# Optimization experiments

Hardware: AMD Instinct MI355X
Metric: run time of the kernel (lower is better)

## Reference

```python
import jax, jax.numpy as jnp
import numpy as np

NUM_HEADS = 6
TAU = 1.0


def _split_heads(y, h):
    b, n, c = y.shape
    return y.reshape(b, n, h, c // h).transpose(0, 2, 1, 3)  # b h n d


def setup_inputs() -> dict:
    key = jax.random.key(0)
    B, M, C = 8, 1026, 384
    names = ["Wq1", "Wq2", "Wk1", "Wk2", "Wv1", "Wv2", "Wo"]
    ks = jax.random.split(key, len(names) + 3)
    inp = {"x": jax.random.normal(ks[0], (B, M, C), jnp.float32)}
    for i, nm in enumerate(names):
        inp[nm] = jax.random.normal(ks[i + 1], (C, C), jnp.float32) * 0.02
        inp["b" + nm[1:]] = jnp.zeros((C,), jnp.float32)
    inp["weights"] = jax.random.normal(ks[-2], (4,), jnp.float32)
    u = jax.random.uniform(ks[-1], (4,), jnp.float32, 1e-6, 1.0 - 1e-6)
    inp["gumbel_noise"] = -jnp.log(-jnp.log(u))  # fixed gumbel sample for determinism
    return inp


def reference(x, Wq1, bq1, Wq2, bq2, Wk1, bk1, Wk2, bk2,
              Wv1, bv1, Wv2, bv2, Wo, bo, weights, gumbel_noise):
    B, M, C = x.shape
    N1 = (M - 2) // 2 + 1  # N + 1, quadrant size
    h = NUM_HEADS
    d = C // h
    scale = d ** -0.5
    x1, x2 = x[:, :N1], x[:, N1:]
    q = jnp.concatenate([_split_heads(x1 @ Wq1 + bq1, h),
                         _split_heads(x2 @ Wq2 + bq2, h)], axis=2)  # b h M d
    k = jnp.concatenate([_split_heads(x1 @ Wk1 + bk1, h),
                         _split_heads(x2 @ Wk2 + bk2, h)], axis=2)
    v1 = _split_heads(x1 @ Wv1 + bv1, h)  # b h N1 d
    v2 = _split_heads(x2 @ Wv2 + bv2, h)
    attn = jnp.einsum('bhqd,bhkd->bhqk', q, k) * scale  # b h M M
    b1 = jax.nn.softmax(attn[:, :, :N1, :N1], axis=-1)
    b2 = jax.nn.softmax(attn[:, :, :N1, N1:], axis=-1)
    b3 = jax.nn.softmax(attn[:, :, N1:, :N1], axis=-1)
    b4 = jax.nn.softmax(attn[:, :, N1:, N1:], axis=-1)
    # hard gumbel-softmax gate (straight-through)
    y_soft = jax.nn.softmax((weights + gumbel_noise) / TAU)
    y_hard = jax.nn.one_hot(jnp.argmax(y_soft), 4, dtype=y_soft.dtype)
    w = y_hard + y_soft - jax.lax.stop_gradient(y_soft)
    A = w[0] * b1 + w[1] * b2 + w[2] * b3 + w[3] * b4  # b h N1 N1
    out1 = jnp.einsum('bhqk,bhkd->bhqd', A, v1)
    out2 = jnp.einsum('bhqk,bhkd->bhqd', A, v2)
    out = jnp.concatenate([out1, out2], axis=2)  # b h M d
    out = out.transpose(0, 2, 1, 3).reshape(B, M, C)
    return out @ Wo + bo
```

## Files before the change

### kernel.cpp

```cpp
#include <hip/hip_runtime.h>

typedef unsigned short u16;
typedef short v8s __attribute__((ext_vector_type(8)));
typedef float v4f __attribute__((ext_vector_type(4)));

namespace {
constexpr int kC = 384;
constexpr int kN1 = 513;
constexpr int kH = 6;
constexpr int kBH = 48;
constexpr int kRows = 4104;
constexpr int kRows2 = 8208;
constexpr int kPld = 576;
constexpr int kTotX = 8208 * 384;
}

#if __has_builtin(__builtin_amdgcn_exp2f)
#define EXP2F(x) __builtin_amdgcn_exp2f(x)
#else
#define EXP2F(x) exp2f(x)
#endif

__device__ __forceinline__ u16 f2b(float f) {
  unsigned int u = __float_as_uint(f);
  u += 0x7fffu + ((u >> 16) & 1u);
  return (u16)(u >> 16);
}

__device__ __forceinline__ float b2f(u16 b) {
  return __uint_as_float(((unsigned)b) << 16);
}

__device__ __forceinline__ int gumbel_argmax(const float* __restrict__ w,
                                             const float* __restrict__ g) {
  float v0 = w[0] + g[0], v1 = w[1] + g[1], v2 = w[2] + g[2], v3 = w[3] + g[3];
  int j = 0;
  float m = v0;
  if (v1 > m) { m = v1; j = 1; }
  if (v2 > m) { m = v2; j = 2; }
  if (v3 > m) { m = v3; j = 3; }
  return j;
}

__global__ __launch_bounds__(256) void prep_w(
    const float* __restrict__ Wq1, const float* __restrict__ Wq2,
    const float* __restrict__ Wk1, const float* __restrict__ Wk2,
    const float* __restrict__ Wv1, const float* __restrict__ Wv2,
    const float* __restrict__ Wo, const float* __restrict__ x,
    const float* __restrict__ wts, const float* __restrict__ gum,
    u16* __restrict__ Wqt, u16* __restrict__ Wkt, u16* __restrict__ Wv1t,
    u16* __restrict__ Wv2t, u16* __restrict__ Wot, u16* __restrict__ xb) {
  const int bx = blockIdx.x;
  if (bx >= 720) {
    const int base = (bx - 720) * 4096 + (int)threadIdx.x * 8;
    for (int p = 0; p < 2; ++p) {
      const int idx = base + p * 2048;
      if (idx < kTotX) {
        const float4 f0 = *(const float4*)(x + idx);
        const float4 f1 = *(const float4*)(x + idx + 4);
        const v8s v = {(short)f2b(f0.x), (short)f2b(f0.y), (short)f2b(f0.z),
                       (short)f2b(f0.w), (short)f2b(f1.x), (short)f2b(f1.y),
                       (short)f2b(f1.z), (short)f2b(f1.w)};
        *(v8s*)(xb + idx) = v;
      }
    }
    return;
  }
  __shared__ float tb[32][33];
  const int z = bx / 144, rem = bx - z * 144;
  const int c0 = (rem % 12) * 32, r0 = (rem / 12) * 32;
  const int j = gumbel_argmax(wts, gum);
  const float* src;
  u16* dst;
  switch (z) {
    case 0: src = (j < 2) ? Wq1 : Wq2; dst = Wqt; break;
    case 1: src = (j == 0 || j == 2) ? Wk1 : Wk2; dst = Wkt; break;
    case 2: src = Wv1; dst = Wv1t; break;
    case 3: src = Wv2; dst = Wv2t; break;
    default: src = Wo; dst = Wot; break;
  }
  const int tx = threadIdx.x & 31, ty = threadIdx.x >> 5;
  for (int p = 0; p < 4; ++p)
    tb[ty + p * 8][tx] = src[(size_t)(r0 + ty + p * 8) * kC + c0 + tx];
  __syncthreads();
  for (int p = 0; p < 4; ++p)
    dst[(size_t)(c0 + ty + p * 8) * kC + r0 + tx] = f2b(tb[tx][ty + p * 8]);
}

__global__ __launch_bounds__(256) void qkv_mfma(
    const u16* __restrict__ xb, const u16* __restrict__ Wqt,
    const u16* __restrict__ Wkt, const u16* __restrict__ Wv1t,
    const u16* __restrict__ Wv2t, const float* __restrict__ bq1,
    const float* __restrict__ bq2, const float* __restrict__ bk1,
    const float* __restrict__ bk2, const float* __restrict__ bv1,
    const float* __restrict__ bv2, const float* __restrict__ wts,
    const float* __restrict__ gum, u16* __restrict__ Qb, u16* __restrict__ Kb,
    u16* __restrict__ Vt1, u16* __restrict__ Vt2) {
  const int bid = blockIdx.x;
  const int xcd = bid & 7;
  const int op = xcd >> 1;
  const int wu = (bid >> 3) * 2 + (xcd & 1);
  if (wu >= 99) return;
  const int mb33 = wu / 3, nb3 = wu - mb33 * 3;

  __shared__ __align__(16) u16 As[128][72];
  __shared__ __align__(16) u16 Bs[128][72];
  const int j = gumbel_argmax(wts, gum);
  const bool vmode = (op >= 2);
  const float* bias;
  int xoff;
  const u16* Wt;
  if (op == 0) {
    bias = (j < 2) ? bq1 : bq2; xoff = (j < 2) ? 0 : kN1; Wt = Wqt;
  } else if (op == 1) {
    const bool u1 = (j == 0 || j == 2);
    bias = u1 ? bk1 : bk2; xoff = u1 ? 0 : kN1; Wt = Wkt;
  } else if (op == 2) {
    bias = bv1; xoff = 0; Wt = Wv1t;
  } else {
    bias = bv2; xoff = kN1; Wt = Wv2t;
  }
  const int m0 = (vmode ? nb3 : mb33) * 128;
  const int n0 = (vmode ? mb33 : nb3) * 128;
  const int tid = threadIdx.x;
  const int lane = tid & 63, l16 = lane & 15, quad = lane >> 4;
  const int wv = tid >> 6, wr = wv >> 1, wc = wv & 1;
  const int sr = tid >> 2, sc = (tid & 3) * 16;

  v4f acc[4][4];
  const v4f z4 = {0.f, 0.f, 0.f, 0.f};
  for (int i = 0; i < 4; ++i)
    for (int n = 0; n < 4; ++n) acc[i][n] = z4;

  const v8s z8 = {0, 0, 0, 0, 0, 0, 0, 0};
  auto prefA = [&](int k0v, int p, v8s& o0, v8s& o1) {
    const int r = p * 64 + sr;
    o0 = z8; o1 = z8;
    if (!vmode) {
      const int t = m0 + r;
      if (t < kRows) {
        const int bb = t / kN1, mm = t - bb * kN1;
        const u16* s = xb + ((size_t)(bb * 1026 + xoff + mm)) * kC + k0v + sc;
        o0 = *(const v8s*)s;
        o1 = *(const v8s*)(s + 8);
      }
    } else {
      const u16* s = Wt + (size_t)(m0 + r) * kC + k0v + sc;
      o0 = *(const v8s*)s;
      o1 = *(const v8s*)(s + 8);
    }
  };
  auto prefB = [&](int k0v, int p, v8s& o0, v8s& o1) {
    const int r = p * 64 + sr;
    o0 = z8; o1 = z8;
    if (!vmode) {
      const u16* s = Wt + (size_t)(n0 + r) * kC + k0v + sc;
      o0 = *(const v8s*)s;
      o1 = *(const v8s*)(s + 8);
    } else {
      const int t = n0 + r;
      if (t < kRows) {
        const int bb = t / kN1, mm = t - bb * kN1;
        const u16* s = xb + ((size_t)(bb * 1026 + xoff + mm)) * kC + k0v + sc;
        o0 = *(const v8s*)s;
        o1 = *(const v8s*)(s + 8);
      }
    }
  };

  v8s a00, a01, a10, a11, b00, b01, b10, b11;
  prefA(0, 0, a00, a01);
  prefA(0, 1, a10, a11);
  prefB(0, 0, b00, b01);
  prefB(0, 1, b10, b11);

  for (int k0 = 0; k0 < kC; k0 += 64) {
    if (k0) __syncthreads();
    *(v8s*)&As[sr][sc] = a00;
    *(v8s*)&As[sr][sc + 8] = a01;
    *(v8s*)&As[64 + sr][sc] = a10;
    *(v8s*)&As[64 + sr][sc + 8] = a11;
    *(v8s*)&Bs[sr][sc] = b00;
    *(v8s*)&Bs[sr][sc + 8] = b01;
    *(v8s*)&Bs[64 + sr][sc] = b10;
    *(v8s*)&Bs[64 + sr][sc + 8] = b11;
    __syncthreads();
    if (k0 + 64 < kC) {
      prefA(k0 + 64, 0, a00, a01);
      prefA(k0 + 64, 1, a10, a11);
      prefB(k0 + 64, 0, b00, b01);
      prefB(k0 + 64, 1, b10, b11);
    }
    for (int ks = 0; ks < 2; ++ks) {
      v8s af[4], bfr[4];
      for (int i = 0; i < 4; ++i)
        af[i] = *(const v8s*)&As[wr * 64 + i * 16 + l16][ks * 32 + quad * 8];
      for (int n = 0; n < 4; ++n)
        bfr[n] = *(const v8s*)&Bs[wc * 64 + n * 16 + l16][ks * 32 + quad * 8];
      for (int i = 0; i < 4; ++i)
        for (int n = 0; n < 4; ++n)
          acc[i][n] = __builtin_amdgcn_mfma_f32_16x16x32_bf16(af[i], bfr[n],
                                                              acc[i][n], 0, 0, 0);
    }
  }

  if (!vmode) {
    u16* outp = (op == 0) ? Qb : Kb;
    const float osc = (op == 0) ? 0.18033688011112042f : 1.0f;
    float bv4[4];
    for (int nt = 0; nt < 4; ++nt) bv4[nt] = bias[n0 + wc * 64 + nt * 16 + l16];
    for (int i = 0; i < 4; ++i) {
      const int rowb = m0 + wr * 64 + i * 16 + quad * 4;
      for (int r = 0; r < 4; ++r) {
        const int row = rowb + r;
        if (row >= kRows) continue;
        for (int nt = 0; nt < 4; ++nt) {
          const int col = n0 + wc * 64 + nt * 16 + l16;
          outp[(size_t)row * kC + col] = f2b((acc[i][nt][r] + bv4[nt]) * osc);
        }
      }
    }
  } else {
    u16* Vt = (op == 2) ? Vt1 : Vt2;
    for (int nt = 0; nt < 4; ++nt) {
      const int t = n0 + wc * 64 + nt * 16 + l16;
      if (t >= kRows) continue;
      const int bb = t / kN1, mm = t - bb * kN1;
      for (int i = 0; i < 4; ++i) {
        const int colb = m0 + wr * 64 + i * 16 + quad * 4;
        for (int r = 0; r < 4; ++r) {
          const int col = colb + r;
          const int hh = col >> 6, d = col & 63;
          Vt[((size_t)(bb * kH + hh) * 64 + d) * kPld + mm] =
              f2b(acc[i][nt][r] + bias[col]);
        }
      }
    }
  }
}

__global__ __launch_bounds__(256) void attn_fused(const u16* __restrict__ Qb,
                                                  const u16* __restrict__ Kb,
                                                  const u16* __restrict__ Vt1,
                                                  const u16* __restrict__ Vt2,
                                                  u16* __restrict__ PRE) {
  __shared__ __align__(16) u16 Ks[64][72];
  __shared__ __align__(16) u16 Vs[128][72];
  __shared__ __align__(16) u16 Ps[4][16][72];
  const int bid = blockIdx.x;
  const int xcd = bid & 7;
  const int t6 = bid >> 3;
  const int bh = xcd * 6 + (t6 % 6);
  const int q0 = (t6 / 6) * 64;
  const int b = bh / kH, hh = bh - b * kH;
  const int tid = threadIdx.x;
  const int w = tid >> 6, lane = tid & 63, l16 = lane & 15, quad = lane >> 4;

  if (q0 == 512) {
    float* Pp = (float*)&Ks[0][0];
    float* Rd = (float*)&Vs[0][0];
    float* wred = (float*)&Ps[0][0];
    v8s q8[8];
    const u16* qs = Qb + ((size_t)(b * kN1 + 512)) * kC + hh * 64;
    for (int c = 0; c < 8; ++c) q8[c] = *(const v8s*)(qs + c * 8);
    for (int k = tid; k < kN1; k += 256) {
      const u16* kr = Kb + ((size_t)(b * kN1 + k)) * kC + hh * 64;
      float s = 0.f;
      for (int c = 0; c < 8; ++c) {
        const v8s kv = *(const v8s*)(kr + c * 8);
        for (int jj = 0; jj < 8; ++jj)
          s += b2f((u16)q8[c][jj]) * b2f((u16)kv[jj]);
      }
      Pp[k] = EXP2F(s);
    }
    __syncthreads();
    float part = 0.f;
    for (int k = tid; k < kN1; k += 256) part += Pp[k];
    for (int o = 1; o < 64; o <<= 1) part += __shfl_xor(part, o);
    if (lane == 0) wred[w] = part;
    __syncthreads();
    const float rinv = 1.f / (wred[0] + wred[1] + wred[2] + wred[3]);
    const int d = tid & 127, half = tid >> 7;
    const u16* vrow = (d < 64) ? (Vt1 + ((size_t)bh * 64 + d) * kPld)
                               : (Vt2 + ((size_t)bh * 64 + (d - 64)) * kPld);
    float acc = 0.f;
    const int kb0 = half * 256;
    for (int k8 = 0; k8 < 256; k8 += 8) {
      const v8s vv = *(const v8s*)(vrow + kb0 + k8);
      for (int jj = 0; jj < 8; ++jj)
        acc += Pp[kb0 + k8 + jj] * b2f((u16)vv[jj]);
    }
    if (half) acc += Pp[512] * b2f(vrow[512]);
    Rd[tid] = acc;
    __syncthreads();
    if (tid < 128) {
      const float o = (Rd[tid] + Rd[tid + 128]) * rinv;
      const int row = b * 1026 + ((d < 64) ? 512 : (kN1 + 512));
      const int col = hh * 64 + (d & 63);
      PRE[(size_t)row * kC + col] = f2b(o);
    }
    return;
  }

  v8s aq0, aq1;
  {
    const int qr = q0 + w * 16 + l16;
    const u16* qs = Qb + ((size_t)(b * kN1 + qr)) * kC + hh * 64 + quad * 8;
    aq0 = *(const v8s*)qs;
    aq1 = *(const v8s*)(qs + 32);
  }
  const int ksr = tid >> 2, ksc = (tid & 3) * 16;
  const int vd = tid >> 1, vc = (tid & 1) * 32;
  const u16* kbase = Kb + (size_t)b * kN1 * kC + hh * 64 + ksc;
  const u16* vbase = ((vd < 64) ? (Vt1 + ((size_t)bh * 64 + vd) * kPld)
                                : (Vt2 + ((size_t)bh * 64 + (vd - 64)) * kPld)) +
                     vc;
  v8s kr0, kr1, vr0, vr1, vr2, vr3;
  {
    const u16* s = kbase + (size_t)ksr * kC;
    kr0 = *(const v8s*)s;
    kr1 = *(const v8s*)(s + 8);
    vr0 = *(const v8s*)(vbase);
    vr1 = *(const v8s*)(vbase + 8);
    vr2 = *(const v8s*)(vbase + 16);
    vr3 = *(const v8s*)(vbase + 24);
  }
  float lsum[4] = {0.f, 0.f, 0.f, 0.f};
  v4f Oacc[8];
  const v4f z4 = {0.f, 0.f, 0.f, 0.f};
  for (int n = 0; n < 8; ++n) Oacc[n] = z4;

  for (int kt = 0; kt < 8; ++kt) {
    const int k0 = kt * 64;
    __syncthreads();
    *(v8s*)&Ks[ksr][ksc] = kr0;
    *(v8s*)&Ks[ksr][ksc + 8] = kr1;
    *(v8s*)&Vs[vd][vc] = vr0;
    *(v8s*)&Vs[vd][vc + 8] = vr1;
    *(v8s*)&Vs[vd][vc + 16] = vr2;
    *(v8s*)&Vs[vd][vc + 24] = vr3;
    __syncthreads();
    if (kt < 7) {
      const u16* s = kbase + (size_t)(k0 + 64 + ksr) * kC;
      kr0 = *(const v8s*)s;
      kr1 = *(const v8s*)(s + 8);
      const u16* t = vbase + k0 + 64;
      vr0 = *(const v8s*)t;
      vr1 = *(const v8s*)(t + 8);
      vr2 = *(const v8s*)(t + 16);
      vr3 = *(const v8s*)(t + 24);
    }
    v4f sacc[4];
    for (int nt = 0; nt < 4; ++nt) sacc[nt] = z4;
    __builtin_amdgcn_s_setprio(1);
    for (int nt = 0; nt < 4; ++nt) {
      const v8s bk0 = *(const v8s*)&Ks[nt * 16 + l16][quad * 8];
      sacc[nt] = __builtin_amdgcn_mfma_f32_16x16x32_bf16(aq0, bk0, sacc[nt], 0, 0, 0);
      const v8s bk1 = *(const v8s*)&Ks[nt * 16 + l16][32 + quad * 8];
      sacc[nt] = __builtin_amdgcn_mfma_f32_16x16x32_bf16(aq1, bk1, sacc[nt], 0, 0, 0);
    }
    __builtin_amdgcn_s_setprio(0);
    for (int r = 0; r < 4; ++r) {
      float ps = 0.f;
      for (int nt = 0; nt < 4; ++nt) {
        const float p = EXP2F(sacc[nt][r]);
        ps += p;
        Ps[w][quad * 4 + r][nt * 16 + l16] = f2b(p);
      }
      lsum[r] += ps;
    }
    __builtin_amdgcn_s_setprio(1);
    for (int kc = 0; kc < 2; ++kc) {
      const v8s ap = *(const v8s*)&Ps[w][l16][kc * 32 + quad * 8];
      for (int n = 0; n < 8; ++n) {
        const v8s bv = *(const v8s*)&Vs[n * 16 + l16][kc * 32 + quad * 8];
        Oacc[n] = __builtin_amdgcn_mfma_f32_16x16x32_bf16(ap, bv, Oacc[n], 0, 0, 0);
      }
    }
    __builtin_amdgcn_s_setprio(0);
  }

  {
    const u16* k512 = Kb + ((size_t)(b * kN1 + 512)) * kC + hh * 64 + quad * 8;
    const v8s kv0 = *(const v8s*)k512;
    const v8s kv1 = *(const v8s*)(k512 + 32);
    float part = 0.f;
    for (int jj = 0; jj < 8; ++jj) {
      part += b2f((u16)aq0[jj]) * b2f((u16)kv0[jj]);
      part += b2f((u16)aq1[jj]) * b2f((u16)kv1[jj]);
    }
    part += __shfl_xor(part, 16);
    part += __shfl_xor(part, 32);
    const float p512 = EXP2F(part);
    float pb[4];
    for (int r = 0; r < 4; ++r) pb[r] = __shfl(p512, quad * 4 + r);
    for (int r = 0; r < 4; ++r) lsum[r] += pb[r] * 0.0625f;
    for (int n = 0; n < 8; ++n) {
      const int d = (n & 3) * 16 + l16;
      const u16* vp = (n < 4) ? (Vt1 + ((size_t)bh * 64 + d) * kPld + 512)
                              : (Vt2 + ((size_t)bh * 64 + d) * kPld + 512);
      const float vv = b2f(*vp);
      for (int r = 0; r < 4; ++r) Oacc[n][r] += pb[r] * vv;
    }
  }

  float rinv[4];
  for (int r = 0; r < 4; ++r) {
    float s = lsum[r];
    for (int o = 1; o <= 8; o <<= 1) s += __shfl_xor(s, o);
    rinv[r] = 1.f / s;
  }
  for (int n = 0; n < 8; ++n) {
    const int col = hh * 64 + (n & 3) * 16 + l16;
    const int rbase = b * 1026 + ((n < 4) ? 0 : kN1);
    for (int r = 0; r < 4; ++r) {
      const int q = q0 + w * 16 + quad * 4 + r;
      PRE[(size_t)(rbase + q) * kC + col] = f2b(Oacc[n][r] * rinv[r]);
    }
  }
}

__global__ __launch_bounds__(256) void out_mfma(const u16* __restrict__ PRE,
                                                const u16* __restrict__ Wot,
                                                const float* __restrict__ bo,
                                                float* __restrict__ OUT) {
  __shared__ __align__(16) u16 As[128][72];
  __shared__ __align__(16) u16 Bs[128][72];
  const int m0 = blockIdx.x * 128, n0 = blockIdx.y * 128;
  const int tid = threadIdx.x;
  const int lane = tid & 63, l16 = lane & 15, quad = lane >> 4;
  const int wv = tid >> 6, wr = wv >> 1, wc = wv & 1;
  const int sr = tid >> 2, sc = (tid & 3) * 16;
  v4f acc[4][4];
  const v4f z4 = {0.f, 0.f, 0.f, 0.f};
  for (int i = 0; i < 4; ++i)
    for (int n = 0; n < 4; ++n) acc[i][n] = z4;

  const v8s z8 = {0, 0, 0, 0, 0, 0, 0, 0};
  auto lA = [&](int k0v, int p, v8s& o0, v8s& o1) {
    const int r = p * 64 + sr;
    o0 = z8; o1 = z8;
    const int row = m0 + r;
    if (row < kRows2) {
      const u16* s = PRE + (size_t)row * kC + k0v + sc;
      o0 = *(const v8s*)s;
      o1 = *(const v8s*)(s + 8);
    }
  };
  auto lB = [&](int k0v, int p, v8s& o0, v8s& o1) {
    const u16* s2 = Wot + (size_t)(n0 + p * 64 + sr) * kC + k0v + sc;
    o0 = *(const v8s*)s2;
    o1 = *(const v8s*)(s2 + 8);
  };

  v8s a00, a01, a10, a11, b00, b01, b10, b11;
  lA(0, 0, a00, a01);
  lA(0, 1, a10, a11);
  lB(0, 0, b00, b01);
  lB(0, 1, b10, b11);

  for (int k0 = 0; k0 < kC; k0 += 64) {
    if (k0) __syncthreads();
    *(v8s*)&As[sr][sc] = a00;
    *(v8s*)&As[sr][sc + 8] = a01;
    *(v8s*)&As[64 + sr][sc] = a10;
    *(v8s*)&As[64 + sr][sc + 8] = a11;
    *(v8s*)&Bs[sr][sc] = b00;
    *(v8s*)&Bs[sr][sc + 8] = b01;
    *(v8s*)&Bs[64 + sr][sc] = b10;
    *(v8s*)&Bs[64 + sr][sc + 8] = b11;
    __syncthreads();
    if (k0 + 64 < kC) {
      lA(k0 + 64, 0, a00, a01);
      lA(k0 + 64, 1, a10, a11);
      lB(k0 + 64, 0, b00, b01);
      lB(k0 + 64, 1, b10, b11);
    }
    for (int ks = 0; ks < 2; ++ks) {
      v8s af[4], bfr[4];
      for (int i = 0; i < 4; ++i)
        af[i] = *(const v8s*)&As[wr * 64 + i * 16 + l16][ks * 32 + quad * 8];
      for (int n = 0; n < 4; ++n)
        bfr[n] = *(const v8s*)&Bs[wc * 64 + n * 16 + l16][ks * 32 + quad * 8];
      for (int i = 0; i < 4; ++i)
        for (int n = 0; n < 4; ++n)
          acc[i][n] = __builtin_amdgcn_mfma_f32_16x16x32_bf16(af[i], bfr[n],
                                                              acc[i][n], 0, 0, 0);
    }
  }
  float bv4[4];
  for (int nt = 0; nt < 4; ++nt) bv4[nt] = bo[n0 + wc * 64 + nt * 16 + l16];
  for (int i = 0; i < 4; ++i) {
    const int rowb = m0 + wr * 64 + i * 16 + quad * 4;
    for (int r = 0; r < 4; ++r) {
      const int row = rowb + r;
      if (row >= kRows2) continue;
      for (int nt = 0; nt < 4; ++nt) {
        const int col = n0 + wc * 64 + nt * 16 + l16;
        OUT[(size_t)row * kC + col] = acc[i][nt][r] + bv4[nt];
      }
    }
  }
}

extern "C" void kernel_launch(void* const* d_in, const int* in_sizes, int n_in,
                              void* d_out, int out_size, void* d_ws,
                              size_t ws_size, hipStream_t stream) {
  const float* x = (const float*)d_in[0];
  const float* Wq1 = (const float*)d_in[1];
  const float* bq1 = (const float*)d_in[2];
  const float* Wq2 = (const float*)d_in[3];
  const float* bq2 = (const float*)d_in[4];
  const float* Wk1 = (const float*)d_in[5];
  const float* bk1 = (const float*)d_in[6];
  const float* Wk2 = (const float*)d_in[7];
  const float* bk2 = (const float*)d_in[8];
  const float* Wv1 = (const float*)d_in[9];
  const float* bv1 = (const float*)d_in[10];
  const float* Wv2 = (const float*)d_in[11];
  const float* bv2 = (const float*)d_in[12];
  const float* Wo = (const float*)d_in[13];
  const float* bo = (const float*)d_in[14];
  const float* wts = (const float*)d_in[15];
  const float* gum = (const float*)d_in[16];
  (void)Wo;

  u16* Wqt = (u16*)d_ws;
  u16* Wkt = Wqt + 147456;
  u16* Wv1t = Wkt + 147456;
  u16* Wv2t = Wv1t + 147456;
  u16* Wot = Wv2t + 147456;
  u16* Qb = Wot + 147456;
  u16* Kb = Qb + (size_t)kRows * kC;
  u16* Vt1 = Kb + (size_t)kRows * kC;
  u16* Vt2 = Vt1 + (size_t)kBH * 64 * kPld;
  u16* PRE = Vt2 + (size_t)kBH * 64 * kPld;
  u16* XB = PRE + (size_t)kRows2 * kC;

  prep_w<<<dim3(1490), 256, 0, stream>>>(Wq1, Wq2, Wk1, Wk2, Wv1, Wv2, Wo, x,
                                         wts, gum, Wqt, Wkt, Wv1t, Wv2t, Wot,
                                         XB);
  qkv_mfma<<<dim3(400), 256, 0, stream>>>(
      XB, Wqt, Wkt, Wv1t, Wv2t, bq1, bq2, bk1, bk2, bv1, bv2, wts, gum, Qb, Kb,
      Vt1, Vt2);
  attn_fused<<<dim3(432), 256, 0, stream>>>(Qb, Kb, Vt1, Vt2, PRE);
  out_mfma<<<dim3(65, 3), 256, 0, stream>>>(PRE, Wot, bo, (float*)d_out);
}
```

Measured before the change: 137.7 us.

## Double-buffer K/V shared-memory tiles in fused attention loop

Splits the K and V shared-memory tiles into two buffers. Each iteration computes on the current buffer and writes the prefetched next tile into the other buffer, so the loop needs one barrier per step instead of two. The aim is to cut barrier stalls and let LDS stores overlap with MFMA work. In exchange, shared memory per block roughly doubles for K/V, which can lower the number of resident blocks per CU.

```diff
diff --git a/kernel.cpp b/kernel.cpp
--- a/kernel.cpp
+++ b/kernel.cpp
@@ -244,8 +244,8 @@
                                                   const u16* __restrict__ Vt1,
                                                   const u16* __restrict__ Vt2,
                                                   u16* __restrict__ PRE) {
-  __shared__ __align__(16) u16 Ks[64][72];
-  __shared__ __align__(16) u16 Vs[128][72];
+  __shared__ __align__(16) u16 Ks[2][64][72];
+  __shared__ __align__(16) u16 Vs[2][128][72];
   __shared__ __align__(16) u16 Ps[4][16][72];
   const int bid = blockIdx.x;
   const int xcd = bid & 7;
@@ -257,9 +257,9 @@
   const int w = tid >> 6, lane = tid & 63, l16 = lane & 15, quad = lane >> 4;
 
   if (q0 == 512) {
-    float* Pp = (float*)&Ks[0][0];
-    float* Rd = (float*)&Vs[0][0];
-    float* wred = (float*)&Ps[0][0];
+    float* Pp = (float*)&Ks[0][0][0];
+    float* Rd = (float*)&Vs[0][0][0];
+    float* wred = (float*)&Ps[0][0][0];
     v8s q8[8];
     const u16* qs = Qb + ((size_t)(b * kN1 + 512)) * kC + hh * 64;
     for (int c = 0; c < 8; ++c) q8[c] = *(const v8s*)(qs + c * 8);
@@ -324,27 +324,28 @@
     vr1 = *(const v8s*)(vbase + 8);
     vr2 = *(const v8s*)(vbase + 16);
     vr3 = *(const v8s*)(vbase + 24);
-  }
+    *(v8s*)&Ks[0][ksr][ksc] = kr0;
+    *(v8s*)&Ks[0][ksr][ksc + 8] = kr1;
+    *(v8s*)&Vs[0][vd][vc] = vr0;
+    *(v8s*)&Vs[0][vd][vc + 8] = vr1;
+    *(v8s*)&Vs[0][vd][vc + 16] = vr2;
+    *(v8s*)&Vs[0][vd][vc + 24] = vr3;
+  }
+  __syncthreads();
+
   float lsum[4] = {0.f, 0.f, 0.f, 0.f};
   v4f Oacc[8];
   const v4f z4 = {0.f, 0.f, 0.f, 0.f};
   for (int n = 0; n < 8; ++n) Oacc[n] = z4;
 
   for (int kt = 0; kt < 8; ++kt) {
-    const int k0 = kt * 64;
-    __syncthreads();
-    *(v8s*)&Ks[ksr][ksc] = kr0;
-    *(v8s*)&Ks[ksr][ksc + 8] = kr1;
-    *(v8s*)&Vs[vd][vc] = vr0;
-    *(v8s*)&Vs[vd][vc + 8] = vr1;
-    *(v8s*)&Vs[vd][vc + 16] = vr2;
-    *(v8s*)&Vs[vd][vc + 24] = vr3;
-    __syncthreads();
+    const int cur = kt & 1;
     if (kt < 7) {
-      const u16* s = kbase + (size_t)(k0 + 64 + ksr) * kC;
+      const int k0n = kt * 64 + 64;
+      const u16* s = kbase + (size_t)(k0n + ksr) * kC;
       kr0 = *(const v8s*)s;
       kr1 = *(const v8s*)(s + 8);
-      const u16* t = vbase + k0 + 64;
+      const u16* t = vbase + k0n;
       vr0 = *(const v8s*)t;
       vr1 = *(const v8s*)(t + 8);
       vr2 = *(const v8s*)(t + 16);
@@ -354,9 +355,9 @@
     for (int nt = 0; nt < 4; ++nt) sacc[nt] = z4;
     __builtin_amdgcn_s_setprio(1);
     for (int nt = 0; nt < 4; ++nt) {
-      const v8s bk0 = *(const v8s*)&Ks[nt * 16 + l16][quad * 8];
+      const v8s bk0 = *(const v8s*)&Ks[cur][nt * 16 + l16][quad * 8];
       sacc[nt] = __builtin_amdgcn_mfma_f32_16x16x32_bf16(aq0, bk0, sacc[nt], 0, 0, 0);
-      const v8s bk1 = *(const v8s*)&Ks[nt * 16 + l16][32 + quad * 8];
+      const v8s bk1 = *(const v8s*)&Ks[cur][nt * 16 + l16][32 + quad * 8];
       sacc[nt] = __builtin_amdgcn_mfma_f32_16x16x32_bf16(aq1, bk1, sacc[nt], 0, 0, 0);
     }
     __builtin_amdgcn_s_setprio(0);
@@ -373,11 +374,20 @@
     for (int kc = 0; kc < 2; ++kc) {
       const v8s ap = *(const v8s*)&Ps[w][l16][kc * 32 + quad * 8];
       for (int n = 0; n < 8; ++n) {
-        const v8s bv = *(const v8s*)&Vs[n * 16 + l16][kc * 32 + quad * 8];
+        const v8s bv = *(const v8s*)&Vs[cur][n * 16 + l16][kc * 32 + quad * 8];
         Oacc[n] = __builtin_amdgcn_mfma_f32_16x16x32_bf16(ap, bv, Oacc[n], 0, 0, 0);
       }
     }
     __builtin_amdgcn_s_setprio(0);
+    if (kt < 7) {
+      *(v8s*)&Ks[cur ^ 1][ksr][ksc] = kr0;
+      *(v8s*)&Ks[cur ^ 1][ksr][ksc + 8] = kr1;
+      *(v8s*)&Vs[cur ^ 1][vd][vc] = vr0;
+      *(v8s*)&Vs[cur ^ 1][vd][vc + 8] = vr1;
+      *(v8s*)&Vs[cur ^ 1][vd][vc + 16] = vr2;
+      *(v8s*)&Vs[cur ^ 1][vd][vc + 24] = vr3;
+      __syncthreads();
+    }
   }
 
   {
```

Measured after the change: 136.5 us. Within noise of the previous version (-0.9%).
